# Optimization experiments

Hardware: AMD Instinct MI355X
Metric: run time of the kernel (lower is better)

Reference implementation:

```python
import jax, jax.numpy as jnp
import numpy as np

C = 64; NET = 32; K = 3; G = 4; GC = C // G; P = K * K
STRIDE = 1; PAD = 1; DIL = 1; OFFSET_SCALE = 1.0
BN_EPS = 1e-5; LN_EPS = 1e-6


def conv2d(x, w, b, groups=1, pad=1):
    # x: (N,C,H,W), w: (O, I//groups, kh, kw)
    y = jax.lax.conv_general_dilated(
        x, w, (1, 1), [(pad, pad), (pad, pad)],
        feature_group_count=groups,
        dimension_numbers=('NCHW', 'OIHW', 'NCHW'))
    return y + b[None, :, None, None]


def dcnv3_core(x, offset, mask):
    """Faithful port of dcnv3_core_pytorch (InternImage).
    x: (N,H,W,C) channels-last; offset: (N,H,W,G*P*2); mask: (N,H,W,G*P) (softmaxed).
    grid_sample(bilinear, zeros padding, align_corners=False) done manually."""
    xp = jnp.pad(x, ((0, 0), (PAD, PAD), (PAD, PAD), (0, 0)))
    N, Hin, Win, _ = xp.shape
    Ho, Wo = offset.shape[1], offset.shape[2]
    # reference points in normalized [0,1] coords (x first, y second)
    start = (DIL * (K - 1)) // 2 + 0.5
    ref_x = (start + jnp.arange(Wo, dtype=jnp.float32) * STRIDE) / Win  # (Wo,)
    ref_y = (start + jnp.arange(Ho, dtype=jnp.float32) * STRIDE) / Hin  # (Ho,)
    ref = jnp.stack(jnp.broadcast_arrays(ref_x[None, :], ref_y[:, None]), axis=-1)  # (Ho,Wo,2)
    # dilation grid (kernel tap offsets, torch meshgrid 'ij' flatten order: w-major)
    kv = (jnp.arange(K, dtype=jnp.float32) * DIL - (DIL * (K - 1)) // 2)
    gx, gy = jnp.meshgrid(kv / Win, kv / Hin, indexing='ij')
    grid = jnp.stack([gx, gy], -1).reshape(P, 2)  # (P,2), same for every group
    # sampling locations, normalized: (N,Ho,Wo,G,P,2)
    off = offset.reshape(N, Ho, Wo, G, P, 2) * (OFFSET_SCALE / jnp.array([Win, Hin], jnp.float32))
    loc = ref[None, :, :, None, None, :] + grid[None, None, None, None, :, :] * OFFSET_SCALE + off
    # grid_sample align_corners=False: pixel = loc*size - 0.5  (since g = 2*loc-1)
    px = loc[..., 0] * Win - 0.5
    py = loc[..., 1] * Hin - 0.5
    x0 = jnp.floor(px); y0 = jnp.floor(py)
    ix0 = x0.astype(jnp.int32); iy0 = y0.astype(jnp.int32)
    wx1 = px - x0; wy1 = py - y0; wx0 = 1.0 - wx1; wy0 = 1.0 - wy1
    xg = xp.reshape(N, Hin, Win, G, GC)
    n_idx = jnp.arange(N)[:, None, None, None, None]
    g_idx = jnp.arange(G)[None, None, None, :, None]

    def sample(ix, iy):
        valid = ((ix >= 0) & (ix < Win) & (iy >= 0) & (iy < Hin)).astype(xg.dtype)
        v = xg[n_idx, jnp.clip(iy, 0, Hin - 1), jnp.clip(ix, 0, Win - 1), g_idx]  # (N,Ho,Wo,G,P,GC)
        return v * valid[..., None]

    val = (sample(ix0, iy0) * (wx0 * wy0)[..., None]
           + sample(ix0 + 1, iy0) * (wx1 * wy0)[..., None]
           + sample(ix0, iy0 + 1) * (wx0 * wy1)[..., None]
           + sample(ix0 + 1, iy0 + 1) * (wx1 * wy1)[..., None])
    out = jnp.einsum('nhwgpc,nhwgp->nhwgc', val, mask.reshape(N, Ho, Wo, G, P))
    return out.reshape(N, Ho, Wo, C)


def setup_inputs() -> dict:
    key = jax.random.key(0)
    ks = jax.random.split(key, 16)
    N, H, W = 4, 128, 128
    f = lambda k, shp, s=1.0: jax.random.normal(k, shp, jnp.float32) * s
    return {
        'input_x': f(ks[0], (N, C, H, W)),
        'input_y': f(ks[1], (N, NET, H, W)),
        'enc_w': f(ks[2], (NET, C), 0.05), 'enc_b': jnp.zeros((NET,), jnp.float32),
        'bn_g': jnp.ones((NET,), jnp.float32), 'bn_b': jnp.zeros((NET,), jnp.float32),
        'bn_m': jnp.zeros((NET,), jnp.float32), 'bn_v': jnp.ones((NET,), jnp.float32),
        'gru_wz': f(ks[3], (NET, 2 * NET, 3, 3), 0.05), 'gru_bz': jnp.zeros((NET,), jnp.float32),
        'gru_wr': f(ks[4], (NET, 2 * NET, 3, 3), 0.05), 'gru_br': jnp.zeros((NET,), jnp.float32),
        'gru_wq': f(ks[5], (NET, 2 * NET, 3, 3), 0.05), 'gru_bq': jnp.zeros((NET,), jnp.float32),
        'dw_w': f(ks[6], (C, 1, 3, 3), 0.1), 'dw_b': jnp.zeros((C,), jnp.float32),
        'ln_g': jnp.ones((C,), jnp.float32), 'ln_b': jnp.zeros((C,), jnp.float32),
        'off_w': f(ks[7], (G * P * 2, C), 0.1), 'off_b': f(ks[8], (G * P * 2,), 0.1),
        'mask_w': f(ks[9], (G * P, C), 0.1), 'mask_b': jnp.zeros((G * P,), jnp.float32),
        'inp_w': f(ks[10], (C, C), 0.1), 'inp_b': jnp.zeros((C,), jnp.float32),
        'out_w': f(ks[11], (C, C), 0.1), 'out_b': jnp.zeros((C,), jnp.float32),
    }


def reference(input_x, input_y, enc_w, enc_b, bn_g, bn_b, bn_m, bn_v,
              gru_wz, gru_bz, gru_wr, gru_br, gru_wq, gru_bq,
              dw_w, dw_b, ln_g, ln_b, off_w, off_b, mask_w, mask_b,
              inp_w, inp_b, out_w, out_b):
    N, _, H, W = input_x.shape
    # encoder: 1x1 Conv + BN(eval) + SiLU
    e = jnp.einsum('nchw,oc->nohw', input_x, enc_w) + enc_b[None, :, None, None]
    e = (e - bn_m[None, :, None, None]) * jax.lax.rsqrt(bn_v + BN_EPS)[None, :, None, None]
    e = e * bn_g[None, :, None, None] + bn_b[None, :, None, None]
    x_en = jax.nn.silu(e)
    # ConvGRU: h' = (1-z)*h + z*q
    hx = jnp.concatenate([input_y, x_en], axis=1)
    z = jax.nn.sigmoid(conv2d(hx, gru_wz, gru_bz))
    r = jax.nn.sigmoid(conv2d(hx, gru_wr, gru_br))
    q = jnp.tanh(conv2d(jnp.concatenate([r * input_y, x_en], axis=1), gru_wq, gru_bq))
    h = (1.0 - z) * input_y + z * q  # (N,NET,H,W)
    # channels-last main path
    inp = input_x.transpose(0, 2, 3, 1)  # (N,H,W,C)
    x = inp @ inp_w.T + inp_b
    # depthwise conv on gru state -> LN (channels_last) -> GELU
    y = conv2d(h, dw_w, dw_b, groups=NET).transpose(0, 2, 3, 1)  # (N,H,W,C)
    mu = y.mean(-1, keepdims=True)
    var = ((y - mu) ** 2).mean(-1, keepdims=True)
    y = (y - mu) * jax.lax.rsqrt(var + LN_EPS) * ln_g + ln_b
    y = jax.nn.gelu(y, approximate=False)
    offset = y @ off_w.T + off_b  # (N,H,W,G*P*2)
    m = y @ mask_w.T + mask_b
    m = jax.nn.softmax(m.reshape(N, H, W, G, P), axis=-1).reshape(N, H, W, G * P)
    x = dcnv3_core(x, offset, m)
    x = x @ out_w.T + out_b
    return jax.nn.silu(x.transpose(0, 3, 1, 2)), h
```

## Files before the change

kernel.cpp:

```cpp
#include <hip/hip_runtime.h>
#include <hip/hip_bf16.h>

typedef __hip_bfloat16 bf16;
typedef short short8v __attribute__((ext_vector_type(8)));
typedef short short4v __attribute__((ext_vector_type(4)));
typedef float float4v __attribute__((ext_vector_type(4)));

static __device__ __forceinline__ float b2f(bf16 v){ return __bfloat162float(v); }
static __device__ __forceinline__ bf16 f2b(float v){ return __float2bfloat16(v); }
static __device__ __forceinline__ float bu2f(unsigned short u){ return __uint_as_float(((unsigned)u) << 16); }
static __device__ __forceinline__ short f2bs(float v){ bf16 t = __float2bfloat16(v); return *(short*)&t; }

#define WT 128
#define HWT 16384

#define OFF_ENC   0
#define OFF_ENCSC 2048
#define OFF_ENCSH 2080
#define OFF_BZ    20544
#define OFF_BR    39008
#define OFF_BQ    57472
#define OFF_DWP   57504
#define OFF_DWB   58080
#define OFF_LNG   58144
#define OFF_LNB   58208
#define OFF_OMB   65184
#define OFF_WINP  65296
#define OFF_BINP  69392
#define OFF_BOUT  73552
#define NW_TOTAL  73616
#define NBF_ZR    36864
#define NBF_Q     18432
#define NBF_OM    7168
#define NBF_OUT   4096
#define NPREP     (NW_TOTAL + NBF_ZR + NBF_Q + NBF_OM + NBF_OUT)
#define NHALO     2064
#define NTOT      (NPREP + NHALO)

#define B_WZRB  294912
#define B_WQB   368640
#define B_WOMB  405504
#define B_WOUTB 419840
#define B_HXP   428544
#define B_QINP  9081344
#define B_ZBUF  17734144
#define B_XL    428544

__global__ void k_prep(
    const float* __restrict__ enc_w, const float* __restrict__ enc_b,
    const float* __restrict__ bn_g, const float* __restrict__ bn_b,
    const float* __restrict__ bn_m, const float* __restrict__ bn_v,
    const float* __restrict__ gwz, const float* __restrict__ gbz,
    const float* __restrict__ gwr, const float* __restrict__ gbr,
    const float* __restrict__ gwq, const float* __restrict__ gbq,
    const float* __restrict__ dww, const float* __restrict__ dwb,
    const float* __restrict__ lng, const float* __restrict__ lnb,
    const float* __restrict__ offw, const float* __restrict__ offb,
    const float* __restrict__ maskw, const float* __restrict__ maskb,
    const float* __restrict__ inpw, const float* __restrict__ inpb,
    const float* __restrict__ outw, const float* __restrict__ outb,
    float* __restrict__ Wp, bf16* __restrict__ wzrb, bf16* __restrict__ wqb,
    bf16* __restrict__ womb, bf16* __restrict__ woutb,
    bf16* __restrict__ hxp, bf16* __restrict__ qinp) {
  int i = blockIdx.x * blockDim.x + threadIdx.x;
  if (i >= NTOT) return;
  if (i >= NPREP) {
    int t = i - NPREP;
    int img = t / 516, r = t % 516;
    int ph, pw;
    if (r < 130) { ph = 0; pw = r; }
    else if (r < 260) { ph = 129; pw = r - 130; }
    else if (r < 388) { ph = r - 260 + 1; pw = 0; }
    else { ph = r - 388 + 1; pw = 129; }
    size_t pb = (((size_t)img * 130 + ph) * 130 + pw) * 64;
    uint4 zz = make_uint4(0, 0, 0, 0);
    #pragma unroll
    for (int k = 0; k < 8; ++k) {
      ((uint4*)(hxp + pb))[k] = zz;
      ((uint4*)(qinp + pb))[k] = zz;
    }
    return;
  }
  if (i >= NW_TOTAL) {
    int d = i - NW_TOTAL;
    if (d < NBF_ZR) {
      int n = d / 576, k = d % 576;
      int tap = k >> 6, cin = k & 63;
      float v = (n < 32) ? gwz[(n*64 + cin)*9 + tap] : gwr[((n-32)*64 + cin)*9 + tap];
      wzrb[d] = f2b(v);
    } else if (d < NBF_ZR + NBF_Q) {
      int d2 = d - NBF_ZR;
      int n = d2 / 576, k = d2 % 576;
      int tap = k >> 6, cin = k & 63;
      wqb[d2] = f2b(gwq[(n*64 + cin)*9 + tap]);
    } else if (d < NBF_ZR + NBF_Q + NBF_OM) {
      int d3 = d - NBF_ZR - NBF_Q;
      int j = d3 >> 6, c = d3 & 63;
      float v = (j < 72) ? offw[j*64 + c] : ((j < 108) ? maskw[(j-72)*64 + c] : 0.f);
      womb[d3] = f2b(v);
    } else {
      int d4 = d - NBF_ZR - NBF_Q - NBF_OM;
      int o = d4 >> 6, c = d4 & 63;
      woutb[d4] = f2b(outw[o*64 + c]);
    }
    return;
  }
  float v;
  if (i < 2048) { int c = i >> 5, o = i & 31; v = enc_w[o*64 + c]; }
  else if (i < 2080) { int o = i - 2048; v = bn_g[o] * rsqrtf(bn_v[o] + 1e-5f); }
  else if (i < 2112) { int o = i - 2080;
    float sc = bn_g[o] * rsqrtf(bn_v[o] + 1e-5f);
    v = (enc_b[o] - bn_m[o]) * sc + bn_b[o]; }
  else if (i < 20544) { v = 0.f; }
  else if (i < 20576) { v = gbz[i - OFF_BZ]; }
  else if (i < 39008) { v = 0.f; }
  else if (i < 39040) { v = gbr[i - OFF_BR]; }
  else if (i < 57472) { v = 0.f; }
  else if (i < 57504) { v = gbq[i - OFF_BQ]; }
  else if (i < 58080) { int d = i - OFF_DWP; int tap = d >> 6, o = d & 63; v = dww[o*9 + tap]; }
  else if (i < 58144) { v = dwb[i - OFF_DWB]; }
  else if (i < 58208) { v = lng[i - OFF_LNG]; }
  else if (i < 58272) { v = lnb[i - OFF_LNB]; }
  else if (i < 65184) { v = 0.f; }
  else if (i < 65292) { int j = i - OFF_OMB; v = (j < 72) ? offb[j] : maskb[j-72]; }
  else if (i < 65296) { v = 0.f; }
  else if (i < 69392) { int d = i - OFF_WINP; int c = d >> 6, o = d & 63; v = inpw[o*64 + c]; }
  else if (i < 69456) { v = inpb[i - OFF_BINP]; }
  else if (i < 73552) { v = 0.f; }
  else { v = outb[i - OFF_BOUT]; }
  Wp[i] = v;
}

__global__ void __launch_bounds__(256) k_pre(
    const float* __restrict__ X, const float* __restrict__ Y,
    const float* __restrict__ Wp, bf16* __restrict__ hxp, bf16* __restrict__ qinp) {
  __shared__ float xls[4096];
  int tid = threadIdx.x;
  int px = tid & 63, sect = tid >> 6;
  int img = blockIdx.z, h = blockIdx.y, w0 = blockIdx.x * 64;
  int hw = h * WT + w0 + px;
  const float* xp = X + (size_t)img * (64 * HWT) + hw;
  #pragma unroll
  for (int i = 0; i < 16; ++i) {
    int c = sect * 16 + i;
    xls[c * 64 + px] = xp[c * HWT];
  }
  const float* yp = Y + (size_t)img * (32 * HWT) + hw;
  bf16 yv[8];
  #pragma unroll
  for (int i = 0; i < 8; ++i) yv[i] = f2b(yp[(sect * 8 + i) * HWT]);
  size_t pb = (((size_t)img * 130 + h + 1) * 130 + (w0 + px + 1)) * 64;
  *(uint4*)(hxp + pb + sect * 8) = *(const uint4*)yv;
  __syncthreads();
  float aen[8];
  #pragma unroll
  for (int o = 0; o < 8; ++o) aen[o] = 0.f;
  for (int k = 0; k < 64; ++k) {
    float a = xls[k * 64 + px];
    const float* we = Wp + OFF_ENC + k * 32 + sect * 8;
    #pragma unroll
    for (int o = 0; o < 8; ++o) aen[o] += a * we[o];
  }
  bf16 xe[8];
  #pragma unroll
  for (int o = 0; o < 8; ++o) {
    int oo = sect * 8 + o;
    float e = aen[o] * Wp[OFF_ENCSC + oo] + Wp[OFF_ENCSH + oo];
    xe[o] = f2b(e / (1.f + __expf(-e)));
  }
  *(uint4*)(hxp + pb + 32 + sect * 8) = *(const uint4*)xe;
  *(uint4*)(qinp + pb + 32 + sect * 8) = *(const uint4*)xe;
}

__global__ void __launch_bounds__(256) k_zr(
    const float* __restrict__ Wp,
    const bf16* __restrict__ hxp, const bf16* __restrict__ wzrb,
    bf16* __restrict__ qinp, bf16* __restrict__ zbuf) {
  __shared__ short zt[32 * 132];
  int tid = threadIdx.x;
  int wv = tid >> 6, ln = tid & 63;
  int quad = ln >> 4, lm = ln & 15;
  int img = blockIdx.z, h = blockIdx.y;
  int p0 = wv * 32;
  const short* hs = (const short*)hxp;
  const short* ws = (const short*)wzrb;
  size_t rowb = ((size_t)img * 130 + h + 1) * 130;
  const short* ab0 = hs + (rowb + p0 + lm + 1) * 64 + quad * 8;
  const short* ab1 = ab0 + 16 * 64;
  int bb = lm * 576 + quad * 8;
  float4v acc[8];
  #pragma unroll
  for (int t = 0; t < 8; ++t) acc[t] = (float4v){0.f, 0.f, 0.f, 0.f};
  #pragma unroll
  for (int kc = 0; kc < 18; ++kc) {
    const int tap = kc >> 1, cin0 = (kc & 1) * 32;
    const int dd = (tap / 3 - 1) * 130 + (tap % 3 - 1);
    short8v a0 = *(const short8v*)(ab0 + dd * 64 + cin0);
    short8v a1 = *(const short8v*)(ab1 + dd * 64 + cin0);
    #pragma unroll
    for (int t = 0; t < 4; ++t) {
      short8v b = *(const short8v*)(ws + bb + t * (16 * 576) + kc * 32);
      acc[t*2]   = __builtin_amdgcn_mfma_f32_16x16x32_bf16(a0, b, acc[t*2], 0, 0, 0);
      acc[t*2+1] = __builtin_amdgcn_mfma_f32_16x16x32_bf16(a1, b, acc[t*2+1], 0, 0, 0);
    }
  }
  #pragma unroll
  for (int mt = 0; mt < 2; ++mt) {
    #pragma unroll
    for (int t = 0; t < 2; ++t) {
      int n = t * 16 + lm;
      float bz = Wp[OFF_BZ + n];
      short zp[4];
      #pragma unroll
      for (int ri = 0; ri < 4; ++ri)
        zp[ri] = f2bs(1.f / (1.f + __expf(-(acc[t*2+mt][ri] + bz))));
      *(short4v*)(zt + n * 132 + p0 + mt * 16 + quad * 4) = *(const short4v*)zp;
    }
  }
  #pragma unroll
  for (int mt = 0; mt < 2; ++mt) {
    #pragma unroll
    for (int t = 2; t < 4; ++t) {
      int c = (t - 2) * 16 + lm;
      float br = Wp[OFF_BR + c];
      #pragma unroll
      for (int ri = 0; ri < 4; ++ri) {
        int px = p0 + mt * 16 + quad * 4 + ri;
        size_t aoff = (rowb + px + 1) * 64 + c;
        float rv = 1.f / (1.f + __expf(-(acc[t*2+mt][ri] + br)));
        float yv = b2f(hxp[aoff]);
        qinp[aoff] = f2b(rv * yv);
      }
    }
  }
  __syncthreads();
  int n2 = tid >> 3, pq = tid & 7;
  short8v z0 = *(const short8v*)(zt + n2 * 132 + pq * 16);
  short8v z1 = *(const short8v*)(zt + n2 * 132 + pq * 16 + 8);
  short* zo = (short*)zbuf + (((size_t)img * 128 + h) * 32 + n2) * 128 + pq * 16;
  *(short8v*)zo = z0;
  *(short8v*)(zo + 8) = z1;
}

__global__ void __launch_bounds__(256) k_qg(
    const float* __restrict__ Y, const float* __restrict__ Wp,
    const bf16* __restrict__ qinp, const bf16* __restrict__ wqb,
    const bf16* __restrict__ zbuf, float* __restrict__ outh) {
  __shared__ float hout[32 * 132];
  int tid = threadIdx.x;
  int wv = tid >> 6, ln = tid & 63;
  int quad = ln >> 4, lm = ln & 15;
  int img = blockIdx.z, h = blockIdx.y;
  int p0 = wv * 32;
  const short* qs = (const short*)qinp;
  const short* ws = (const short*)wqb;
  size_t rowb = ((size_t)img * 130 + h + 1) * 130;
  const short* ab0 = qs + (rowb + p0 + lm + 1) * 64 + quad * 8;
  const short* ab1 = ab0 + 16 * 64;
  int bb = lm * 576 + quad * 8;
  float4v acc[4];
  #pragma unroll
  for (int t = 0; t < 4; ++t) acc[t] = (float4v){0.f, 0.f, 0.f, 0.f};
  #pragma unroll
  for (int kc = 0; kc < 18; ++kc) {
    const int tap = kc >> 1, cin0 = (kc & 1) * 32;
    const int dd = (tap / 3 - 1) * 130 + (tap % 3 - 1);
    short8v a0 = *(const short8v*)(ab0 + dd * 64 + cin0);
    short8v a1 = *(const short8v*)(ab1 + dd * 64 + cin0);
    #pragma unroll
    for (int t = 0; t < 2; ++t) {
      short8v b = *(const short8v*)(ws + bb + t * (16 * 576) + kc * 32);
      acc[t*2]   = __builtin_amdgcn_mfma_f32_16x16x32_bf16(a0, b, acc[t*2], 0, 0, 0);
      acc[t*2+1] = __builtin_amdgcn_mfma_f32_16x16x32_bf16(a1, b, acc[t*2+1], 0, 0, 0);
    }
  }
  #pragma unroll
  for (int mt = 0; mt < 2; ++mt) {
    #pragma unroll
    for (int t = 0; t < 2; ++t) {
      int n = t * 16 + lm;
      float bq = Wp[OFF_BQ + n];
      float4 hv;
      hv.x = acc[t*2+mt][0] + bq; hv.y = acc[t*2+mt][1] + bq;
      hv.z = acc[t*2+mt][2] + bq; hv.w = acc[t*2+mt][3] + bq;
      *(float4*)(hout + n * 132 + p0 + mt * 16 + quad * 4) = hv;
    }
  }
  __syncthreads();
  const short* zbb = (const short*)zbuf + ((size_t)img * 128 + h) * 32 * 128;
  #pragma unroll
  for (int r = 0; r < 4; ++r) {
    int n = (tid >> 5) + r * 8;
    int px4 = (tid & 31) * 4;
    float4 hv = *(const float4*)(hout + n * 132 + px4);
    uint2 zz = *(const uint2*)(zbb + n * 128 + px4);
    size_t gb = ((size_t)img * 32 + n) * HWT + h * 128 + px4;
    float4 yv = *(const float4*)(Y + gb);
    float z0 = bu2f((unsigned short)(zz.x & 0xFFFFu)), z1 = bu2f((unsigned short)(zz.x >> 16));
    float z2 = bu2f((unsigned short)(zz.y & 0xFFFFu)), z3 = bu2f((unsigned short)(zz.y >> 16));
    float4 o;
    o.x = (1.f - z0) * yv.x + z0 * tanhf(hv.x);
    o.y = (1.f - z1) * yv.y + z1 * tanhf(hv.y);
    o.z = (1.f - z2) * yv.z + z2 * tanhf(hv.z);
    o.w = (1.f - z3) * yv.w + z3 * tanhf(hv.w);
    *(float4*)(outh + gb) = o;
  }
}

__global__ void __launch_bounds__(256) k_xl(
    const float* __restrict__ X, const float* __restrict__ Wp, bf16* __restrict__ xl) {
  __shared__ float xls[4096];
  int tid = threadIdx.x;
  int px = tid & 63, sect = tid >> 6;
  int img = blockIdx.z, h = blockIdx.y, w0 = blockIdx.x * 64;
  int hw = h * WT + w0 + px;
  const float* xp = X + (size_t)img * (64 * HWT) + hw;
  #pragma unroll
  for (int i = 0; i < 16; ++i) {
    int c = sect * 16 + i;
    xls[c * 64 + px] = xp[c * HWT];
  }
  __syncthreads();
  float acc[16];
  #pragma unroll
  for (int o = 0; o < 16; ++o) acc[o] = Wp[OFF_BINP + sect * 16 + o];
  for (int k = 0; k < 64; ++k) {
    float a = xls[k * 64 + px];
    const float* wr = Wp + OFF_WINP + k * 64 + sect * 16;
    #pragma unroll
    for (int o = 0; o < 16; ++o) acc[o] += a * wr[o];
  }
  bf16 ov[16];
  #pragma unroll
  for (int o = 0; o < 16; ++o) ov[o] = f2b(acc[o]);
  bf16* op = xl + ((size_t)img * HWT + hw) * 64 + sect * 16;
  ((uint4*)op)[0] = ((const uint4*)ov)[0];
  ((uint4*)op)[1] = ((const uint4*)ov)[1];
}

#define LDS_PSA  0
#define LDS_PSB  2048
#define LDS_STAT 4096
#define LDS_Y    4608
#define LDS_OM   13824
#define LDS_TOT  42752

__global__ void __launch_bounds__(512) k_mega(
    const float* __restrict__ Wp, const float* __restrict__ hb,
    const bf16* __restrict__ xl, const bf16* __restrict__ womb,
    const bf16* __restrict__ woutb, float* __restrict__ out0) {
  __shared__ char smem[LDS_TOT];
  float* psa  = (float*)(smem + LDS_PSA);
  float* psb  = (float*)(smem + LDS_PSB);
  float* stat = (float*)(smem + LDS_STAT);
  short* yls  = (short*)(smem + LDS_Y);
  float* omls = (float*)(smem + LDS_OM);
  short* vls  = (short*)(smem + LDS_Y);

  int tid = threadIdx.x;
  int img = blockIdx.z, h = blockIdx.y, w0 = blockIdx.x * 64;

  int wloc = tid & 63, part = tid >> 6;
  int w = w0 + wloc;
  float yv[8];
  {
    const float* hn = hb + (size_t)img * (32 * HWT);
    #pragma unroll
    for (int i = 0; i < 8; ++i) yv[i] = Wp[OFF_DWB + part*8 + i];
    #pragma unroll
    for (int tap = 0; tap < 9; ++tap) {
      int dy = tap / 3 - 1, dx = tap % 3 - 1;
      int hh = h + dy, ww = w + dx;
      bool ok = ((unsigned)hh < 128u) && ((unsigned)ww < 128u);
      int off = hh * WT + ww;
      #pragma unroll
      for (int j = 0; j < 4; ++j) {
        int cin = part * 4 + j;
        float a = ok ? hn[cin * HWT + off] : 0.f;
        yv[2*j]   += a * Wp[OFF_DWP + tap*64 + part*8 + 2*j];
        yv[2*j+1] += a * Wp[OFF_DWP + tap*64 + part*8 + 2*j+1];
      }
    }
  }
  float lsum = 0.f, lsq = 0.f;
  #pragma unroll
  for (int i = 0; i < 8; ++i) { lsum += yv[i]; lsq += yv[i]*yv[i]; }
  psa[part * 64 + wloc] = lsum;
  psb[part * 64 + wloc] = lsq;
  __syncthreads();
  if (tid < 64) {
    float s = 0.f, q = 0.f;
    #pragma unroll
    for (int p = 0; p < 8; ++p) { s += psa[p*64 + tid]; q += psb[p*64 + tid]; }
    float mu = s * (1.f/64.f);
    float var = q * (1.f/64.f) - mu * mu;
    stat[tid*2] = mu;
    stat[tid*2+1] = rsqrtf(var + 1e-6f);
  }
  __syncthreads();
  {
    float mu = stat[wloc*2], inv = stat[wloc*2+1];
    bf16 tmp[8];
    #pragma unroll
    for (int i = 0; i < 8; ++i) {
      int c = part*8 + i;
      float v = (yv[i] - mu) * inv * Wp[OFF_LNG + c] + Wp[OFF_LNB + c];
      tmp[i] = f2b(0.5f * v * (1.f + erff(v * 0.70710678118654752f)));
    }
    *(short8v*)(yls + wloc*72 + part*8) = *(const short8v*)tmp;
  }
  __syncthreads();

  int wv = tid >> 6, ln = tid & 63, quad = ln >> 4, lm = ln & 15;
  if (wv < 7) {
    const short* wb = (const short*)womb;
    float4v acc[4];
    #pragma unroll
    for (int mt = 0; mt < 4; ++mt) acc[mt] = (float4v){0.f,0.f,0.f,0.f};
    #pragma unroll
    for (int kc = 0; kc < 2; ++kc) {
      short8v b = *(const short8v*)(wb + (wv*16 + lm)*64 + kc*32 + quad*8);
      #pragma unroll
      for (int mt = 0; mt < 4; ++mt) {
        short8v a = *(const short8v*)(yls + (mt*16 + lm)*72 + kc*32 + quad*8);
        acc[mt] = __builtin_amdgcn_mfma_f32_16x16x32_bf16(a, b, acc[mt], 0, 0, 0);
      }
    }
    float bias = Wp[OFF_OMB + wv*16 + lm];
    #pragma unroll
    for (int mt = 0; mt < 4; ++mt) {
      #pragma unroll
      for (int ri = 0; ri < 4; ++ri)
        omls[(mt*16 + quad*4 + ri)*113 + wv*16 + lm] = acc[mt][ri] + bias;
    }
  }
  __syncthreads();

  {
    int px = tid >> 3, g = (tid >> 1) & 3, half = tid & 1;
    const float* oml = omls + px*113;
    float m[9];
    #pragma unroll
    for (int p = 0; p < 9; ++p) m[p] = oml[72 + g*9 + p];
    float mx = m[0];
    #pragma unroll
    for (int p = 1; p < 9; ++p) mx = fmaxf(mx, m[p]);
    float sum = 0.f;
    #pragma unroll
    for (int p = 0; p < 9; ++p) { m[p] = __expf(m[p] - mx); sum += m[p]; }
    float rs = 1.f / sum;
    int wg = w0 + px;
    const bf16* xn = xl + (size_t)img * (HWT * 64);
    float acc[8];
    #pragma unroll
    for (int i = 0; i < 8; ++i) acc[i] = 0.f;
    for (int p = 0; p < 9; ++p) {
      float bx = (float)(wg + p / 3 - 1);
      float by = (float)(h + p % 3 - 1);
      float ox = oml[g*18 + p*2];
      float oy = oml[g*18 + p*2 + 1];
      float mk = m[p] * rs;
      float pxx = bx + ox, pyy = by + oy;
      float fx = floorf(pxx), fy = floorf(pyy);
      int jx0 = (int)fx, jy0 = (int)fy;
      float wx1 = pxx - fx, wy1 = pyy - fy;
      float wx0 = 1.f - wx1, wy0 = 1.f - wy1;
      int cjx[4] = { jx0, jx0 + 1, jx0, jx0 + 1 };
      int cjy[4] = { jy0, jy0, jy0 + 1, jy0 + 1 };
      float cw[4] = { wx0*wy0, wx1*wy0, wx0*wy1, wx1*wy1 };
      #pragma unroll
      for (int k = 0; k < 4; ++k) {
        if ((unsigned)cjx[k] < 128u && (unsigned)cjy[k] < 128u) {
          float cf = mk * cw[k];
          const bf16* s = xn + (size_t)(cjy[k] * WT + cjx[k]) * 64 + g * 16 + half * 8;
          uint4 u0 = *(const uint4*)(s);
          const unsigned uu[4] = {u0.x,u0.y,u0.z,u0.w};
          #pragma unroll
          for (int q = 0; q < 4; ++q) {
            acc[2*q]     += cf * bu2f((unsigned short)(uu[q] & 0xFFFFu));
            acc[2*q + 1] += cf * bu2f((unsigned short)(uu[q] >> 16));
          }
        }
      }
    }
    bf16 tmp[8];
    #pragma unroll
    for (int i = 0; i < 8; ++i) tmp[i] = f2b(acc[i]);
    *(short8v*)(vls + px*72 + g*16 + half*8) = *(const short8v*)tmp;
  }
  __syncthreads();

  if (wv < 4) {
    const short* wb = (const short*)woutb;
    float4v acc[4];
    #pragma unroll
    for (int mt = 0; mt < 4; ++mt) acc[mt] = (float4v){0.f,0.f,0.f,0.f};
    #pragma unroll
    for (int kc = 0; kc < 2; ++kc) {
      short8v b = *(const short8v*)(wb + (wv*16 + lm)*64 + kc*32 + quad*8);
      #pragma unroll
      for (int mt = 0; mt < 4; ++mt) {
        short8v a = *(const short8v*)(vls + (mt*16 + lm)*72 + kc*32 + quad*8);
        acc[mt] = __builtin_amdgcn_mfma_f32_16x16x32_bf16(a, b, acc[mt], 0, 0, 0);
      }
    }
    int ch = wv*16 + lm;
    float bias = Wp[OFF_BOUT + ch];
    #pragma unroll
    for (int mt = 0; mt < 4; ++mt) {
      float4 v;
      float s0 = acc[mt][0] + bias; v.x = s0 / (1.f + __expf(-s0));
      float s1 = acc[mt][1] + bias; v.y = s1 / (1.f + __expf(-s1));
      float s2 = acc[mt][2] + bias; v.z = s2 / (1.f + __expf(-s2));
      float s3 = acc[mt][3] + bias; v.w = s3 / (1.f + __expf(-s3));
      *(float4*)(out0 + ((size_t)img*64 + ch)*HWT + h*128 + w0 + mt*16 + quad*4) = v;
    }
  }
}

extern "C" void kernel_launch(void* const* d_in, const int* in_sizes, int n_in,
                              void* d_out, int out_size, void* d_ws, size_t ws_size,
                              hipStream_t stream) {
  const float* input_x = (const float*)d_in[0];
  const float* input_y = (const float*)d_in[1];

  float* Wp = (float*)d_ws;
  bf16* WZRB  = (bf16*)((char*)d_ws + B_WZRB);
  bf16* WQB   = (bf16*)((char*)d_ws + B_WQB);
  bf16* WOMB  = (bf16*)((char*)d_ws + B_WOMB);
  bf16* WOUTB = (bf16*)((char*)d_ws + B_WOUTB);
  bf16* HXP   = (bf16*)((char*)d_ws + B_HXP);
  bf16* QINP  = (bf16*)((char*)d_ws + B_QINP);
  bf16* ZBUF  = (bf16*)((char*)d_ws + B_ZBUF);
  bf16* XL    = (bf16*)((char*)d_ws + B_XL);
  float* out0 = (float*)d_out;
  float* outh = (float*)d_out + 4194304;

  k_prep<<<dim3((NTOT + 255)/256), dim3(256), 0, stream>>>(
      (const float*)d_in[2], (const float*)d_in[3], (const float*)d_in[4], (const float*)d_in[5],
      (const float*)d_in[6], (const float*)d_in[7], (const float*)d_in[8], (const float*)d_in[9],
      (const float*)d_in[10], (const float*)d_in[11], (const float*)d_in[12], (const float*)d_in[13],
      (const float*)d_in[14], (const float*)d_in[15], (const float*)d_in[16], (const float*)d_in[17],
      (const float*)d_in[18], (const float*)d_in[19], (const float*)d_in[20], (const float*)d_in[21],
      (const float*)d_in[22], (const float*)d_in[23], (const float*)d_in[24], (const float*)d_in[25],
      Wp, WZRB, WQB, WOMB, WOUTB, HXP, QINP);
  k_pre<<<dim3(2, 128, 4), dim3(256), 0, stream>>>(input_x, input_y, Wp, HXP, QINP);
  k_zr <<<dim3(1, 128, 4), dim3(256), 0, stream>>>(Wp, HXP, WZRB, QINP, ZBUF);
  k_qg <<<dim3(1, 128, 4), dim3(256), 0, stream>>>(input_y, Wp, QINP, WQB, ZBUF, outh);
  k_xl <<<dim3(2, 128, 4), dim3(256), 0, stream>>>(input_x, Wp, XL);
  k_mega<<<dim3(2, 128, 4), dim3(512), 0, stream>>>(Wp, outh, XL, WOMB, WOUTB, out0);
}
```

Before: 271.6 us.

## Preload conv operands, stage r*h writes through LDS, store offsets/mask as bf16

In the z/r and q GRU conv kernels, all 18 A-operand fragments are loaded into registers up front, before the MFMA loop, so global load latency overlaps. The r*y product is staged in shared memory and written to qinp as coalesced 16-byte vectors instead of scattered 2-byte stores. In the mega kernel the offset/mask logits are kept in LDS as bf16 rather than fp32, shrinking LDS use to allow more resident blocks. That precision drop on sampling offsets may change numerics, and the larger register footprint from the preloads may lower occupancy.

Result: no change. 273.4 us (+0.7%).

```diff
diff --git a/kernel.cpp b/kernel.cpp
--- a/kernel.cpp
+++ b/kernel.cpp
@@ -177,6 +177,7 @@
     const bf16* __restrict__ hxp, const bf16* __restrict__ wzrb,
     bf16* __restrict__ qinp, bf16* __restrict__ zbuf) {
   __shared__ short zt[32 * 132];
+  __shared__ short ryt[128 * 40];
   int tid = threadIdx.x;
   int wv = tid >> 6, ln = tid & 63;
   int quad = ln >> 4, lm = ln & 15;
@@ -188,20 +189,24 @@
   const short* ab0 = hs + (rowb + p0 + lm + 1) * 64 + quad * 8;
   const short* ab1 = ab0 + 16 * 64;
   int bb = lm * 576 + quad * 8;
-  float4v acc[8];
-  #pragma unroll
-  for (int t = 0; t < 8; ++t) acc[t] = (float4v){0.f, 0.f, 0.f, 0.f};
+  short8v a0[18], a1[18];
   #pragma unroll
   for (int kc = 0; kc < 18; ++kc) {
     const int tap = kc >> 1, cin0 = (kc & 1) * 32;
     const int dd = (tap / 3 - 1) * 130 + (tap % 3 - 1);
-    short8v a0 = *(const short8v*)(ab0 + dd * 64 + cin0);
-    short8v a1 = *(const short8v*)(ab1 + dd * 64 + cin0);
+    a0[kc] = *(const short8v*)(ab0 + dd * 64 + cin0);
+    a1[kc] = *(const short8v*)(ab1 + dd * 64 + cin0);
+  }
+  float4v acc[8];
+  #pragma unroll
+  for (int t = 0; t < 8; ++t) acc[t] = (float4v){0.f, 0.f, 0.f, 0.f};
+  #pragma unroll
+  for (int kc = 0; kc < 18; ++kc) {
     #pragma unroll
     for (int t = 0; t < 4; ++t) {
       short8v b = *(const short8v*)(ws + bb + t * (16 * 576) + kc * 32);
-      acc[t*2]   = __builtin_amdgcn_mfma_f32_16x16x32_bf16(a0, b, acc[t*2], 0, 0, 0);
-      acc[t*2+1] = __builtin_amdgcn_mfma_f32_16x16x32_bf16(a1, b, acc[t*2+1], 0, 0, 0);
+      acc[t*2]   = __builtin_amdgcn_mfma_f32_16x16x32_bf16(a0[kc], b, acc[t*2], 0, 0, 0);
+      acc[t*2+1] = __builtin_amdgcn_mfma_f32_16x16x32_bf16(a1[kc], b, acc[t*2+1], 0, 0, 0);
     }
   }
   #pragma unroll
@@ -226,20 +231,29 @@
       #pragma unroll
       for (int ri = 0; ri < 4; ++ri) {
         int px = p0 + mt * 16 + quad * 4 + ri;
-        size_t aoff = (rowb + px + 1) * 64 + c;
         float rv = 1.f / (1.f + __expf(-(acc[t*2+mt][ri] + br)));
-        float yv = b2f(hxp[aoff]);
-        qinp[aoff] = f2b(rv * yv);
+        float yy = b2f(hxp[(rowb + px + 1) * 64 + c]);
+        ryt[px * 40 + c] = f2bs(rv * yy);
       }
     }
   }
   __syncthreads();
-  int n2 = tid >> 3, pq = tid & 7;
-  short8v z0 = *(const short8v*)(zt + n2 * 132 + pq * 16);
-  short8v z1 = *(const short8v*)(zt + n2 * 132 + pq * 16 + 8);
-  short* zo = (short*)zbuf + (((size_t)img * 128 + h) * 32 + n2) * 128 + pq * 16;
-  *(short8v*)zo = z0;
-  *(short8v*)(zo + 8) = z1;
+  {
+    int n2 = tid >> 3, pq = tid & 7;
+    short8v z0 = *(const short8v*)(zt + n2 * 132 + pq * 16);
+    short8v z1 = *(const short8v*)(zt + n2 * 132 + pq * 16 + 8);
+    short* zo = (short*)zbuf + (((size_t)img * 128 + h) * 32 + n2) * 128 + pq * 16;
+    *(short8v*)zo = z0;
+    *(short8v*)(zo + 8) = z1;
+  }
+  {
+    int px = tid >> 1, chalf = tid & 1;
+    short8v r0 = *(const short8v*)(ryt + px * 40 + chalf * 16);
+    short8v r1 = *(const short8v*)(ryt + px * 40 + chalf * 16 + 8);
+    short* qo = (short*)qinp + (rowb + px + 1) * 64 + chalf * 16;
+    *(short8v*)qo = r0;
+    *(short8v*)(qo + 8) = r1;
+  }
 }
 
 __global__ void __launch_bounds__(256) k_qg(
@@ -258,20 +272,24 @@
   const short* ab0 = qs + (rowb + p0 + lm + 1) * 64 + quad * 8;
   const short* ab1 = ab0 + 16 * 64;
   int bb = lm * 576 + quad * 8;
-  float4v acc[4];
-  #pragma unroll
-  for (int t = 0; t < 4; ++t) acc[t] = (float4v){0.f, 0.f, 0.f, 0.f};
+  short8v a0[18], a1[18];
   #pragma unroll
   for (int kc = 0; kc < 18; ++kc) {
     const int tap = kc >> 1, cin0 = (kc & 1) * 32;
     const int dd = (tap / 3 - 1) * 130 + (tap % 3 - 1);
-    short8v a0 = *(const short8v*)(ab0 + dd * 64 + cin0);
-    short8v a1 = *(const short8v*)(ab1 + dd * 64 + cin0);
+    a0[kc] = *(const short8v*)(ab0 + dd * 64 + cin0);
+    a1[kc] = *(const short8v*)(ab1 + dd * 64 + cin0);
+  }
+  float4v acc[4];
+  #pragma unroll
+  for (int t = 0; t < 4; ++t) acc[t] = (float4v){0.f, 0.f, 0.f, 0.f};
+  #pragma unroll
+  for (int kc = 0; kc < 18; ++kc) {
     #pragma unroll
     for (int t = 0; t < 2; ++t) {
       short8v b = *(const short8v*)(ws + bb + t * (16 * 576) + kc * 32);
-      acc[t*2]   = __builtin_amdgcn_mfma_f32_16x16x32_bf16(a0, b, acc[t*2], 0, 0, 0);
-      acc[t*2+1] = __builtin_amdgcn_mfma_f32_16x16x32_bf16(a1, b, acc[t*2+1], 0, 0, 0);
+      acc[t*2]   = __builtin_amdgcn_mfma_f32_16x16x32_bf16(a0[kc], b, acc[t*2], 0, 0, 0);
+      acc[t*2+1] = __builtin_amdgcn_mfma_f32_16x16x32_bf16(a1[kc], b, acc[t*2+1], 0, 0, 0);
     }
   }
   #pragma unroll
@@ -343,7 +361,7 @@
 #define LDS_STAT 4096
 #define LDS_Y    4608
 #define LDS_OM   13824
-#define LDS_TOT  42752
+#define LDS_TOT  28416
 
 __global__ void __launch_bounds__(512) k_mega(
     const float* __restrict__ Wp, const float* __restrict__ hb,
@@ -354,7 +372,7 @@
   float* psb  = (float*)(smem + LDS_PSB);
   float* stat = (float*)(smem + LDS_STAT);
   short* yls  = (short*)(smem + LDS_Y);
-  float* omls = (float*)(smem + LDS_OM);
+  short* omls = (short*)(smem + LDS_OM);
   short* vls  = (short*)(smem + LDS_Y);
 
   int tid = threadIdx.x;
@@ -431,17 +449,17 @@
     for (int mt = 0; mt < 4; ++mt) {
       #pragma unroll
       for (int ri = 0; ri < 4; ++ri)
-        omls[(mt*16 + quad*4 + ri)*113 + wv*16 + lm] = acc[mt][ri] + bias;
+        omls[(mt*16 + quad*4 + ri)*114 + wv*16 + lm] = f2bs(acc[mt][ri] + bias);
     }
   }
   __syncthreads();
 
   {
     int px = tid >> 3, g = (tid >> 1) & 3, half = tid & 1;
-    const float* oml = omls + px*113;
+    const short* oml = omls + px*114;
     float m[9];
     #pragma unroll
-    for (int p = 0; p < 9; ++p) m[p] = oml[72 + g*9 + p];
+    for (int p = 0; p < 9; ++p) m[p] = bu2f((unsigned short)oml[72 + g*9 + p]);
     float mx = m[0];
     #pragma unroll
     for (int p = 1; p < 9; ++p) mx = fmaxf(mx, m[p]);
@@ -457,8 +475,8 @@
     for (int p = 0; p < 9; ++p) {
       float bx = (float)(wg + p / 3 - 1);
       float by = (float)(h + p % 3 - 1);
-      float ox = oml[g*18 + p*2];
-      float oy = oml[g*18 + p*2 + 1];
+      float ox = bu2f((unsigned short)oml[g*18 + p*2]);
+      float oy = bu2f((unsigned short)oml[g*18 + p*2 + 1]);
       float mk = m[p] * rs;
       float pxx = bx + ox, pyy = by + oy;
       float fx = floorf(pxx), fy = floorf(pyy);
```
